# Kernel tuning notes

Measured on AMD Instinct MI355X. Metric: run time of the kernel, lower is better.

The kernel has to match this reference:

```python
import jax, jax.numpy as jnp
import numpy as np

V, N, C, H, W = 4, 65536, 128, 512, 512
M_POOL, K, DH = 1024, 5, 128


def setup_inputs() -> dict:
    key = jax.random.key(0)
    ks = jax.random.split(key, 6)
    points = jax.random.normal(ks[0], (N, 3), dtype=jnp.float32) * 0.3  # human-scale pcd near origin
    zbuffer = 2.0 + jax.random.uniform(ks[1], (V, 1, H, W), dtype=jnp.float32)  # depth ~ camera distance
    feat_map = jax.random.normal(ks[2], (V, C, H, W), dtype=jnp.float32) * 0.1
    image = jax.random.uniform(ks[3], (V, 3, H, W), dtype=jnp.float32)
    # cameras: identity rotation, small x-baseline, looking at origin from z=2.5
    R = jnp.tile(jnp.eye(3, dtype=jnp.float32)[None], (V, 1, 1))
    t = jnp.stack([jnp.array([0.1 * v - 0.15, 0.0, 2.5], dtype=jnp.float32) for v in range(V)])
    extr = jnp.concatenate([R, t[:, :, None]], axis=-1)  # [V,3,4]
    intr = jnp.tile(jnp.array([[700.0, 0.0, W / 2], [0.0, 700.0, H / 2], [0.0, 0.0, 1.0]], dtype=jnp.float32)[None], (V, 1, 1))
    W1 = jax.random.normal(ks[4], (C + 1, DH), dtype=jnp.float32) * 0.05
    b1 = jnp.zeros((DH,), dtype=jnp.float32)
    w2 = jax.random.normal(ks[5], (DH, 1), dtype=jnp.float32) * 0.05
    return dict(points=points, extr=extr, intr=intr, zbuffer=zbuffer,
                feat_map=feat_map, image=image, W1=W1, b1=b1, w2=w2)


def _bilinear(img, u, v):
    """Zero-padded bilinear sample. img [C,H,W]; u,v [N] pixel coords -> [N,C]."""
    Cc, Hh, Ww = img.shape
    u0f = jnp.floor(u); v0f = jnp.floor(v)
    du = u - u0f; dv = v - v0f
    u0 = u0f.astype(jnp.int32); v0 = v0f.astype(jnp.int32)
    out = jnp.zeros((Cc, u.shape[0]), dtype=img.dtype)
    for vi, ui, w in ((v0, u0, (1 - du) * (1 - dv)), (v0, u0 + 1, du * (1 - dv)),
                      (v0 + 1, u0, (1 - du) * dv), (v0 + 1, u0 + 1, du * dv)):
        valid = ((vi >= 0) & (vi < Hh) & (ui >= 0) & (ui < Ww)).astype(img.dtype)
        vals = img[:, jnp.clip(vi, 0, Hh - 1), jnp.clip(ui, 0, Ww - 1)]  # [C,N]
        out = out + vals * (w * valid)[None]
    return out.T  # [N,C]


def _project(points, extr, intr):
    cam = jnp.einsum('vij,nj->vni', extr[:, :, :3], points) + extr[:, None, :, 3]  # [V,N,3]
    depth = cam[..., 2]  # [V,N]
    pix = jnp.einsum('vij,vnj->vni', intr, cam)
    u = pix[..., 0] / (pix[..., 2] + 1e-9)
    v = pix[..., 1] / (pix[..., 2] + 1e-9)
    return u, v, depth


def reference(points, extr, intr, zbuffer, feat_map, image, W1, b1, w2):
    u, v, depth = _project(points, extr, intr)
    sample = jax.vmap(_bilinear)  # over V views
    zbuf = sample(zbuffer, u, v)[..., 0]  # [V,N] sampled z-buffer (0 outside frame)
    out_mask = jnp.any(zbuf == 0.0, axis=0)  # [N] point missing in some view
    # --- KNN inverse-distance zbuf replacement (torch.no_grad block) ---
    pts_sg = jax.lax.stop_gradient(points)
    zbuf_sg = jax.lax.stop_gradient(zbuf)
    cand = pts_sg[:M_POOL]                       # candidate in-point pool
    cand_bad = out_mask[:M_POOL]
    d2 = jnp.sum((pts_sg[:, None, :] - cand[None, :, :]) ** 2, axis=-1)  # [N,M]
    d2 = jnp.where(cand_bad[None, :], jnp.inf, d2)
    negd, idx = jax.lax.top_k(-d2, K)            # K nearest candidates
    dists = jnp.sqrt(jnp.maximum(-negd, 0.0))
    disp = 1.0 / (dists + 1e-8)
    wknn = disp / (jnp.sum(disp, -1, keepdims=True) + 1e-12)  # [N,K]
    replace = jnp.sum(zbuf_sg[:, idx] * wknn[None], -1)       # [V,N]
    zbuf = jnp.where(out_mask[None], replace, zbuf)
    # --- visibility ---
    vis = 1.0 - jnp.abs(zbuf - depth) / (zbuf + 1e-9)  # [V,N]
    # --- multi-view projector sampling + attention fusion (MVF) ---
    feat_s = sample(feat_map, u, v)  # [V,N,C]
    rgb_s = sample(image, u, v)      # [V,N,3]
    x = jnp.concatenate([feat_s, vis[..., None]], -1)          # [V,N,C+1]
    h = jax.nn.relu(jnp.einsum('vnc,cd->vnd', x, W1) + b1)     # [V,N,DH]
    attn = jax.nn.softmax(jnp.einsum('vnd,do->vno', h, w2), axis=0)  # softmax over views
    feat = jnp.sum(attn * feat_s, axis=0)  # [N,C]
    rgb = jnp.sum(attn * rgb_s, axis=0)    # [N,3]
    return jnp.concatenate([feat, rgb], axis=-1)  # [N,C+3]
```

## Files before the change

kernel.cpp:

```cpp
#include <hip/hip_runtime.h>
#include <math.h>

#define NV 4
#define NPT 65536
#define NC 128
#define IMH 512
#define IMW 512
#define MPOOL 1024
#define NDH 128
#define KNN 5
#define NB 8
#define OUTC 131

typedef unsigned int uint32;
typedef unsigned short ushort16;
typedef __attribute__((ext_vector_type(8))) short short8v;
typedef __attribute__((ext_vector_type(4))) float float4v;

__device__ inline ushort16 f2bf(float f) {
    uint32 u = __float_as_uint(f);
    u += 0x7fffu + ((u >> 16) & 1u);
    return (ushort16)(u >> 16);
}
__device__ inline float bflo(uint32 a) { return __uint_as_float(a << 16); }
__device__ inline float bfhi(uint32 a) { return __uint_as_float(a & 0xffff0000u); }
__device__ inline float bf1(ushort16 a) { return __uint_as_float(((uint32)a) << 16); }

__global__ void k_wprep(const float* __restrict__ W1, uint4* __restrict__ Bf,
                        int* __restrict__ counter) {
    int idx = blockIdx.x * blockDim.x + threadIdx.x;
    if (idx == 0) *counter = 0;
    if (idx >= 5 * 8 * 64) return;
    int l = idx & 63, t = (idx >> 6) & 7, kb = idx >> 9;
    int d = t * 16 + (l & 15);
    uint32 w[4];
#pragma unroll
    for (int p = 0; p < 4; ++p) {
        uint32 lohi = 0;
#pragma unroll
        for (int h = 0; h < 2; ++h) {
            int j = p * 2 + h;
            int k = kb * 32 + (l >> 4) * 8 + j;
            float wv = (k < NC + 1) ? W1[k * NDH + d] : 0.f;
            lohi |= ((uint32)f2bf(wv)) << (16 * h);
        }
        w[p] = lohi;
    }
    Bf[idx] = make_uint4(w[0], w[1], w[2], w[3]);
}

__global__ __launch_bounds__(256)
void k_prep(const float* __restrict__ pts, const float* __restrict__ extr,
            const float* __restrict__ intr, const float* __restrict__ zbuffer,
            float* __restrict__ uarr, float* __restrict__ varr,
            float* __restrict__ darr, float* __restrict__ zarr,
            int* __restrict__ mask, int* __restrict__ list,
            int* __restrict__ counter) {
    int n = blockIdx.x * blockDim.x + threadIdx.x;
    if (n >= NPT) return;
    float p0 = pts[3 * n], p1 = pts[3 * n + 1], p2 = pts[3 * n + 2];
    int msk = 0;
#pragma unroll
    for (int v = 0; v < NV; ++v) {
        const float* e = extr + v * 12;
        float c0 = e[0] * p0 + e[1] * p1 + e[2] * p2 + e[3];
        float c1 = e[4] * p0 + e[5] * p1 + e[6] * p2 + e[7];
        float c2 = e[8] * p0 + e[9] * p1 + e[10] * p2 + e[11];
        const float* kk = intr + v * 9;
        float x0 = kk[0] * c0 + kk[1] * c1 + kk[2] * c2;
        float x1 = kk[3] * c0 + kk[4] * c1 + kk[5] * c2;
        float x2 = kk[6] * c0 + kk[7] * c1 + kk[8] * c2;
        float uu = x0 / (x2 + 1e-9f);
        float vv = x1 / (x2 + 1e-9f);
        int vn = v * NPT + n;
        uarr[vn] = uu; varr[vn] = vv; darr[vn] = c2;

        const float* img = zbuffer + (size_t)v * IMH * IMW;
        float u0f = floorf(uu), v0f = floorf(vv);
        float du = uu - u0f, dv = vv - v0f;
        int iu0 = (int)u0f, iv0 = (int)v0f;
        float w00 = (1.f - du) * (1.f - dv);
        float w01 = du * (1.f - dv);
        float w10 = (1.f - du) * dv;
        float w11 = du * dv;
        int iu0c = min(max(iu0, 0), IMW - 1), iu1c = min(max(iu0 + 1, 0), IMW - 1);
        int iv0c = min(max(iv0, 0), IMH - 1), iv1c = min(max(iv0 + 1, 0), IMH - 1);
        float m00 = (iu0 >= 0 && iu0 < IMW && iv0 >= 0 && iv0 < IMH) ? w00 : 0.f;
        float m01 = (iu0 + 1 >= 0 && iu0 + 1 < IMW && iv0 >= 0 && iv0 < IMH) ? w01 : 0.f;
        float m10 = (iu0 >= 0 && iu0 < IMW && iv0 + 1 >= 0 && iv0 + 1 < IMH) ? w10 : 0.f;
        float m11 = (iu0 + 1 >= 0 && iu0 + 1 < IMW && iv0 + 1 >= 0 && iv0 + 1 < IMH) ? w11 : 0.f;
        float z = img[iv0c * IMW + iu0c] * m00 + img[iv0c * IMW + iu1c] * m01 +
                  img[iv1c * IMW + iu0c] * m10 + img[iv1c * IMW + iu1c] * m11;
        zarr[vn] = z;
        msk |= (z == 0.f);
    }
    mask[n] = msk;
    if (msk) {
        int pos = atomicAdd(counter, 1);
        list[pos] = n;
    }
}

__global__ __launch_bounds__(256)
void k_knn_c(const float* __restrict__ pts, const int* __restrict__ mask,
             const int* __restrict__ list, const int* __restrict__ counter,
             float* __restrict__ zarr) {
    __shared__ float cx[MPOOL], cy[MPOOL], cz[MPOOL];
    int count = *counter;
    if ((int)blockIdx.x * 256 >= count) return;
    for (int m = threadIdx.x; m < MPOOL; m += 256) {
        int bad = mask[m];
        cx[m] = bad ? INFINITY : pts[3 * m];
        cy[m] = pts[3 * m + 1];
        cz[m] = pts[3 * m + 2];
    }
    __syncthreads();
    int i = blockIdx.x * 256 + threadIdx.x;
    if (i >= count) return;
    int n = list[i];
    float px = pts[3 * n], py = pts[3 * n + 1], pz = pts[3 * n + 2];
    float bd[KNN];
    int bi[KNN];
#pragma unroll
    for (int k = 0; k < KNN; ++k) { bd[k] = INFINITY; bi[k] = 0; }
    for (int m = 0; m < MPOOL; ++m) {
        float dx = px - cx[m];
        float dy = py - cy[m];
        float dz = pz - cz[m];
        float d = dx * dx + dy * dy + dz * dz;
        int id = m;
#pragma unroll
        for (int k = 0; k < KNN; ++k) {
            if (d < bd[k]) {
                float td = bd[k]; int ti = bi[k];
                bd[k] = d; bi[k] = id;
                d = td; id = ti;
            }
        }
    }
    float disp[KNN];
    float s = 0.f;
#pragma unroll
    for (int k = 0; k < KNN; ++k) {
        float dist = sqrtf(fmaxf(bd[k], 0.f));
        disp[k] = 1.f / (dist + 1e-8f);
        s += disp[k];
    }
    float inv = 1.f / (s + 1e-12f);
#pragma unroll
    for (int v = 0; v < NV; ++v) {
        float r = 0.f;
#pragma unroll
        for (int k = 0; k < KNN; ++k) r += zarr[v * NPT + bi[k]] * (disp[k] * inv);
        zarr[v * NPT + n] = r;
    }
}

__global__ __launch_bounds__(256)
void k_tfeat(const float* __restrict__ feat, ushort16* __restrict__ tfeat) {
    __shared__ ushort16 tile[128][130];
    int bid = blockIdx.x;
    int xt = bid & 3;
    int y = (bid >> 2) & 511;
    int v = bid >> 11;
    int x0 = xt * 128;
    int lane = threadIdx.x & 63, wave = threadIdx.x >> 6;
    int half = lane >> 5, l5 = lane & 31;
    const size_t HW = (size_t)IMH * IMW;
    const float* src = feat + (size_t)v * NC * HW + (size_t)y * IMW + x0;
#pragma unroll
    for (int i = 0; i < 16; ++i) {
        int c = i * 8 + wave * 2 + half;
        float4 val = *(const float4*)(src + (size_t)c * HW + l5 * 4);
        int px = l5 * 4;
        tile[px + 0][c] = f2bf(val.x);
        tile[px + 1][c] = f2bf(val.y);
        tile[px + 2][c] = f2bf(val.z);
        tile[px + 3][c] = f2bf(val.w);
    }
    __syncthreads();
    uint32* dst = (uint32*)tfeat + ((size_t)v * HW + (size_t)y * IMW + x0) * 64;
#pragma unroll
    for (int i = 0; i < 32; ++i) {
        int pix = i * 4 + wave;
        uint32 val = *(const uint32*)&tile[pix][2 * lane];
        dst[(size_t)pix * 64 + lane] = val;
    }
}

__global__ __launch_bounds__(128)
void k_fused_m(const float* __restrict__ uarr, const float* __restrict__ varr,
               const float* __restrict__ darr, const float* __restrict__ zarr,
               const ushort16* __restrict__ tfeat, const float* __restrict__ image,
               const uint4* __restrict__ Bf, const float* __restrict__ b1,
               const float* __restrict__ w2, float* __restrict__ out) {
    const int tid = threadIdx.x;
    const int n0 = blockIdx.x * NB;
    const size_t HW = (size_t)IMH * IMW;
    __shared__ ushort16 fs[32][168];
    __shared__ float rgbs[32][3];
    __shared__ int po[32][4];
    __shared__ float pm[32][4];
    __shared__ float sc[32];
    __shared__ float red[32][2];

    {
        int q = tid >> 2, corner = tid & 3;
        int nb = q >> 2, v = q & 3;
        int vn = v * NPT + n0 + nb;
        float uu = uarr[vn], vv = varr[vn];
        float u0f = floorf(uu), v0f = floorf(vv);
        float du = uu - u0f, dv = vv - v0f;
        int iu0 = (int)u0f, iv0 = (int)v0f;
        float w00 = (1.f - du) * (1.f - dv);
        float w01 = du * (1.f - dv);
        float w10 = (1.f - du) * dv;
        float w11 = du * dv;
        int iu0c = min(max(iu0, 0), IMW - 1), iu1c = min(max(iu0 + 1, 0), IMW - 1);
        int iv0c = min(max(iv0, 0), IMH - 1), iv1c = min(max(iv0 + 1, 0), IMH - 1);
        float m00 = (iu0 >= 0 && iu0 < IMW && iv0 >= 0 && iv0 < IMH) ? w00 : 0.f;
        float m01 = (iu0 + 1 < IMW && iu0 + 1 >= 0 && iv0 >= 0 && iv0 < IMH) ? w01 : 0.f;
        float m10 = (iu0 >= 0 && iu0 < IMW && iv0 + 1 < IMH && iv0 + 1 >= 0) ? w10 : 0.f;
        float m11 = (iu0 + 1 < IMW && iu0 + 1 >= 0 && iv0 + 1 < IMH && iv0 + 1 >= 0) ? w11 : 0.f;
        int iuc, ivc;
        float mm;
        if (corner == 0)      { ivc = iv0c; iuc = iu0c; mm = m00; }
        else if (corner == 1) { ivc = iv0c; iuc = iu1c; mm = m01; }
        else if (corner == 2) { ivc = iv1c; iuc = iu0c; mm = m10; }
        else                  { ivc = iv1c; iuc = iu1c; mm = m11; }
        int oo = ivc * IMW + iuc;
        po[q][corner] = oo;
        pm[q][corner] = mm;
        const float* ib = image + (size_t)v * 3 * HW + oo;
        float cr = ib[0] * mm, cg = ib[HW] * mm, cb = ib[2 * HW] * mm;
        cr += __shfl_xor(cr, 1); cr += __shfl_xor(cr, 2);
        cg += __shfl_xor(cg, 1); cg += __shfl_xor(cg, 2);
        cb += __shfl_xor(cb, 1); cb += __shfl_xor(cb, 2);
        if (corner == 0) {
            rgbs[q][0] = cr; rgbs[q][1] = cg; rgbs[q][2] = cb;
            float z = zarr[vn], dd = darr[vn];
            float vis = 1.f - fabsf(z - dd) / (z + 1e-9f);
            fs[q][128] = f2bf(vis);
        }
        for (int k = 129 + corner; k < 168; k += 4) fs[q][k] = 0;
    }
    __syncthreads();

    const uint32* T = (const uint32*)tfeat;
    {
        int wv = tid >> 6, l = tid & 63;
        int ql = l >> 4, g = l & 15;
#pragma unroll
        for (int i = 0; i < 4; ++i) {
            int q = i * 8 + wv * 4 + ql;
            int v = q & 3;
            const uint32* Bv = T + (size_t)v * HW * 64;
            float a0 = 0.f, a1 = 0.f, a2 = 0.f, a3 = 0.f;
            float a4 = 0.f, a5 = 0.f, a6 = 0.f, a7 = 0.f;
#pragma unroll
            for (int k = 0; k < 4; ++k) {
                uint4 A = *(const uint4*)(Bv + (size_t)po[q][k] * 64 + g * 4);
                float m = pm[q][k];
                a0 += bflo(A.x) * m; a1 += bfhi(A.x) * m;
                a2 += bflo(A.y) * m; a3 += bfhi(A.y) * m;
                a4 += bflo(A.z) * m; a5 += bfhi(A.z) * m;
                a6 += bflo(A.w) * m; a7 += bfhi(A.w) * m;
            }
            uint4 r;
            r.x = (uint32)f2bf(a0) | ((uint32)f2bf(a1) << 16);
            r.y = (uint32)f2bf(a2) | ((uint32)f2bf(a3) << 16);
            r.z = (uint32)f2bf(a4) | ((uint32)f2bf(a5) << 16);
            r.w = (uint32)f2bf(a6) | ((uint32)f2bf(a7) << 16);
            *(uint4*)&fs[q][g * 8] = r;
        }
    }
    __syncthreads();

    const int l = tid & 63, w = tid >> 6;
    const int col = l & 15, kg = l >> 4;
    float4v acc[2][4];
#pragma unroll
    for (int g = 0; g < 2; ++g)
#pragma unroll
        for (int t = 0; t < 4; ++t) acc[g][t] = (float4v){0.f, 0.f, 0.f, 0.f};
#pragma unroll
    for (int kb = 0; kb < 5; ++kb) {
        short8v a0 = *(const short8v*)&fs[col][kb * 32 + kg * 8];
        short8v a1 = *(const short8v*)&fs[16 + col][kb * 32 + kg * 8];
#pragma unroll
        for (int tt = 0; tt < 4; ++tt) {
            int t = w * 4 + tt;
            short8v bv = *(const short8v*)&Bf[(kb * 8 + t) * 64 + l];
            acc[0][tt] = __builtin_amdgcn_mfma_f32_16x16x32_bf16(a0, bv, acc[0][tt], 0, 0, 0);
            acc[1][tt] = __builtin_amdgcn_mfma_f32_16x16x32_bf16(a1, bv, acc[1][tt], 0, 0, 0);
        }
    }
    float bias[4], w2v[4];
#pragma unroll
    for (int tt = 0; tt < 4; ++tt) {
        int d = (w * 4 + tt) * 16 + col;
        bias[tt] = b1[d];
        w2v[tt] = w2[d];
    }
    float p[2][4] = {{0.f, 0.f, 0.f, 0.f}, {0.f, 0.f, 0.f, 0.f}};
#pragma unroll
    for (int g = 0; g < 2; ++g)
#pragma unroll
        for (int tt = 0; tt < 4; ++tt)
#pragma unroll
            for (int r = 0; r < 4; ++r)
                p[g][r] += fmaxf(acc[g][tt][r] + bias[tt], 0.f) * w2v[tt];
#pragma unroll
    for (int m = 1; m < 16; m <<= 1)
#pragma unroll
        for (int g = 0; g < 2; ++g)
#pragma unroll
            for (int r = 0; r < 4; ++r) p[g][r] += __shfl_xor(p[g][r], m);
    if (col == 0) {
#pragma unroll
        for (int g = 0; g < 2; ++g)
#pragma unroll
            for (int r = 0; r < 4; ++r) red[g * 16 + kg * 4 + r][w] = p[g][r];
    }
    __syncthreads();
    if (tid < 32) sc[tid] = red[tid][0] + red[tid][1];
    __syncthreads();
    if (tid < NB) {
        float s0 = sc[tid * 4 + 0], s1 = sc[tid * 4 + 1];
        float s2 = sc[tid * 4 + 2], s3 = sc[tid * 4 + 3];
        float mx = fmaxf(fmaxf(s0, s1), fmaxf(s2, s3));
        float e0 = expf(s0 - mx), e1 = expf(s1 - mx);
        float e2 = expf(s2 - mx), e3 = expf(s3 - mx);
        float inv = 1.f / (e0 + e1 + e2 + e3);
        sc[tid * 4 + 0] = e0 * inv; sc[tid * 4 + 1] = e1 * inv;
        sc[tid * 4 + 2] = e2 * inv; sc[tid * 4 + 3] = e3 * inv;
    }
    __syncthreads();

#pragma unroll
    for (int nb = 0; nb < NB; ++nb) {
        int n = n0 + nb;
        float f = 0.f;
#pragma unroll
        for (int v = 0; v < NV; ++v) f += sc[nb * 4 + v] * bf1(fs[nb * 4 + v][tid]);
        out[(size_t)n * OUTC + tid] = f;
        if (tid < 3) {
            float r = 0.f;
#pragma unroll
            for (int v = 0; v < NV; ++v) r += sc[nb * 4 + v] * rgbs[nb * 4 + v][tid];
            out[(size_t)n * OUTC + NC + tid] = r;
        }
    }
}

__global__ __launch_bounds__(128)
void k_fused_d(const float* __restrict__ uarr, const float* __restrict__ varr,
               const float* __restrict__ darr, const float* __restrict__ zarr,
               const float* __restrict__ feat, const float* __restrict__ image,
               const float* __restrict__ W1, const float* __restrict__ b1,
               const float* __restrict__ w2, float* __restrict__ out) {
    const int tid = threadIdx.x;
    const int n0 = blockIdx.x * 4;
    __shared__ float fs[4][NV][NC];
    __shared__ float rgbs[4][NV][3];
    __shared__ float sc[4][NV];
    __shared__ float red[4][NV][2];
    float vis[4][NV];

#pragma unroll
    for (int nb = 0; nb < 4; ++nb) {
        int n = n0 + nb;
#pragma unroll
        for (int v = 0; v < NV; ++v) {
            int vn = v * NPT + n;
            float uu = uarr[vn], vv = varr[vn];
            float u0f = floorf(uu), v0f = floorf(vv);
            float du = uu - u0f, dv = vv - v0f;
            int iu0 = (int)u0f, iv0 = (int)v0f;
            float w00 = (1.f - du) * (1.f - dv);
            float w01 = du * (1.f - dv);
            float w10 = (1.f - du) * dv;
            float w11 = du * dv;
            int iu0c = min(max(iu0, 0), IMW - 1), iu1c = min(max(iu0 + 1, 0), IMW - 1);
            int iv0c = min(max(iv0, 0), IMH - 1), iv1c = min(max(iv0 + 1, 0), IMH - 1);
            float m00 = (iu0 >= 0 && iu0 < IMW && iv0 >= 0 && iv0 < IMH) ? w00 : 0.f;
            float m01 = (iu0 + 1 < IMW && iu0 + 1 >= 0 && iv0 >= 0 && iv0 < IMH) ? w01 : 0.f;
            float m10 = (iu0 >= 0 && iu0 < IMW && iv0 + 1 < IMH && iv0 + 1 >= 0) ? w10 : 0.f;
            float m11 = (iu0 + 1 < IMW && iu0 + 1 >= 0 && iv0 + 1 < IMH && iv0 + 1 >= 0) ? w11 : 0.f;
            int o00 = iv0c * IMW + iu0c, o01 = iv0c * IMW + iu1c;
            int o10 = iv1c * IMW + iu0c, o11 = iv1c * IMW + iu1c;
            const float* base = feat + ((size_t)(v * NC + tid)) * IMH * IMW;
            fs[nb][v][tid] = base[o00] * m00 + base[o01] * m01 +
                             base[o10] * m10 + base[o11] * m11;
            if (tid < 3) {
                const float* ib = image + ((size_t)(v * 3 + tid)) * IMH * IMW;
                rgbs[nb][v][tid] = ib[o00] * m00 + ib[o01] * m01 +
                                   ib[o10] * m10 + ib[o11] * m11;
            }
            float z = zarr[vn], dd = darr[vn];
            vis[nb][v] = 1.f - fabsf(z - dd) / (z + 1e-9f);
        }
    }
    __syncthreads();

    float h[4][NV];
    float bv = b1[tid];
#pragma unroll
    for (int nb = 0; nb < 4; ++nb)
#pragma unroll
        for (int v = 0; v < NV; ++v) h[nb][v] = bv;
    for (int c = 0; c < NC; ++c) {
        float w = W1[c * NDH + tid];
#pragma unroll
        for (int nb = 0; nb < 4; ++nb)
#pragma unroll
            for (int v = 0; v < NV; ++v) h[nb][v] = fmaf(fs[nb][v][c], w, h[nb][v]);
    }
    {
        float w = W1[NC * NDH + tid];
#pragma unroll
        for (int nb = 0; nb < 4; ++nb)
#pragma unroll
            for (int v = 0; v < NV; ++v) h[nb][v] = fmaf(vis[nb][v], w, h[nb][v]);
    }
    float w2t = w2[tid];
    int lane = tid & 63, wave = tid >> 6;
#pragma unroll
    for (int nb = 0; nb < 4; ++nb) {
#pragma unroll
        for (int v = 0; v < NV; ++v) {
            float p = fmaxf(h[nb][v], 0.f) * w2t;
#pragma unroll
            for (int off = 32; off > 0; off >>= 1) p += __shfl_down(p, off);
            if (lane == 0) red[nb][v][wave] = p;
        }
    }
    __syncthreads();
    if (tid < 16) {
        int nb = tid >> 2, v = tid & 3;
        sc[nb][v] = red[nb][v][0] + red[nb][v][1];
    }
    __syncthreads();
    if (tid < 4) {
        float s0 = sc[tid][0], s1 = sc[tid][1], s2 = sc[tid][2], s3 = sc[tid][3];
        float mx = fmaxf(fmaxf(s0, s1), fmaxf(s2, s3));
        float e0 = expf(s0 - mx), e1 = expf(s1 - mx);
        float e2 = expf(s2 - mx), e3 = expf(s3 - mx);
        float inv = 1.f / (e0 + e1 + e2 + e3);
        sc[tid][0] = e0 * inv; sc[tid][1] = e1 * inv;
        sc[tid][2] = e2 * inv; sc[tid][3] = e3 * inv;
    }
    __syncthreads();
#pragma unroll
    for (int nb = 0; nb < 4; ++nb) {
        int n = n0 + nb;
        float f = 0.f;
#pragma unroll
        for (int v = 0; v < NV; ++v) f += sc[nb][v] * fs[nb][v][tid];
        out[(size_t)n * OUTC + tid] = f;
        if (tid < 3) {
            float r = 0.f;
#pragma unroll
            for (int v = 0; v < NV; ++v) r += sc[nb][v] * rgbs[nb][v][tid];
            out[(size_t)n * OUTC + NC + tid] = r;
        }
    }
}

extern "C" void kernel_launch(void* const* d_in, const int* in_sizes, int n_in,
                              void* d_out, int out_size, void* d_ws, size_t ws_size,
                              hipStream_t stream) {
    const float* pts = (const float*)d_in[0];
    const float* extr = (const float*)d_in[1];
    const float* intr = (const float*)d_in[2];
    const float* zbuffer = (const float*)d_in[3];
    const float* feat = (const float*)d_in[4];
    const float* image = (const float*)d_in[5];
    const float* W1 = (const float*)d_in[6];
    const float* b1 = (const float*)d_in[7];
    const float* w2 = (const float*)d_in[8];
    float* out = (float*)d_out;

    const size_t VN = (size_t)NV * NPT;
    float* uarr = (float*)d_ws;
    float* varr = uarr + VN;
    float* darr = varr + VN;
    float* zarr = darr + VN;
    int* mask = (int*)(zarr + VN);
    int* list = mask + NPT;
    int* counter = list + NPT;
    uint4* Bf = (uint4*)(counter + 16);
    char* after = (char*)(Bf + 5 * 8 * 64);
    ushort16* tfeat = (ushort16*)after;
    size_t need = (size_t)((char*)tfeat - (char*)d_ws) + (size_t)NV * IMH * IMW * NC * 2;

    k_wprep<<<10, 256, 0, stream>>>(W1, Bf, counter);
    k_prep<<<NPT / 256, 256, 0, stream>>>(pts, extr, intr, zbuffer,
                                          uarr, varr, darr, zarr,
                                          mask, list, counter);
    k_knn_c<<<NPT / 256, 256, 0, stream>>>(pts, mask, list, counter, zarr);

    if (ws_size >= need) {
        k_tfeat<<<NV * 512 * 4, 256, 0, stream>>>(feat, tfeat);
        k_fused_m<<<NPT / NB, 128, 0, stream>>>(uarr, varr, darr, zarr, tfeat, image,
                                                Bf, b1, w2, out);
    } else {
        k_fused_d<<<NPT / 4, 128, 0, stream>>>(uarr, varr, darr, zarr, feat, image,
                                               W1, b1, w2, out);
    }
}
```

Measured before the change: 472.2 us.

## Split fused sampling kernel into per-view transpose+MLP passes and a final fusion kernel

Restructures the fast path so each view is transposed to bf16 and then immediately sampled and scored by an MLP kernel, one view at a time. The aim is to keep each view's transposed feature map hot in the large cache while it is gathered, instead of gathering across all four views' 128 MB of transposed data. Sampled features and scores go to new workspace buffers, and a final kernel does the softmax, the weighted sum and the RGB sampling. This adds global writes and reads of the intermediate features (about 64 MB bf16 each way), extra kernel launches, and a larger workspace requirement. If the workspace is too small, the code falls back to the direct kernel.

```diff
diff --git a/kernel.cpp b/kernel.cpp
--- a/kernel.cpp
+++ b/kernel.cpp
@@ -9,7 +9,6 @@
 #define MPOOL 1024
 #define NDH 128
 #define KNN 5
-#define NB 8
 #define OUTC 131
 
 typedef unsigned int uint32;
@@ -157,12 +156,12 @@
 }
 
 __global__ __launch_bounds__(256)
-void k_tfeat(const float* __restrict__ feat, ushort16* __restrict__ tfeat) {
+void k_tfeat_v(const float* __restrict__ feat, ushort16* __restrict__ tfeat,
+               int v) {
     __shared__ ushort16 tile[128][130];
     int bid = blockIdx.x;
     int xt = bid & 3;
-    int y = (bid >> 2) & 511;
-    int v = bid >> 11;
+    int y = bid >> 2;
     int x0 = xt * 128;
     int lane = threadIdx.x & 63, wave = threadIdx.x >> 6;
     int half = lane >> 5, l5 = lane & 31;
@@ -189,20 +188,142 @@
 }
 
 __global__ __launch_bounds__(128)
-void k_fused_m(const float* __restrict__ uarr, const float* __restrict__ varr,
-               const float* __restrict__ darr, const float* __restrict__ zarr,
-               const ushort16* __restrict__ tfeat, const float* __restrict__ image,
-               const uint4* __restrict__ Bf, const float* __restrict__ b1,
-               const float* __restrict__ w2, float* __restrict__ out) {
+void k_mlp_v(const float* __restrict__ uarr, const float* __restrict__ varr,
+             const float* __restrict__ darr, const float* __restrict__ zarr,
+             const ushort16* __restrict__ tfeat, const uint4* __restrict__ Bf,
+             const float* __restrict__ b1, const float* __restrict__ w2,
+             ushort16* __restrict__ fsb, float* __restrict__ sbuf, int v) {
     const int tid = threadIdx.x;
-    const int n0 = blockIdx.x * NB;
+    const int n0 = blockIdx.x * 32;
     const size_t HW = (size_t)IMH * IMW;
     __shared__ ushort16 fs[32][168];
-    __shared__ float rgbs[32][3];
     __shared__ int po[32][4];
     __shared__ float pm[32][4];
+    __shared__ float red[32][2];
+
+    {
+        int q = tid >> 2, corner = tid & 3;
+        int vn = v * NPT + n0 + q;
+        float uu = uarr[vn], vv = varr[vn];
+        float u0f = floorf(uu), v0f = floorf(vv);
+        float du = uu - u0f, dv = vv - v0f;
+        int iu0 = (int)u0f, iv0 = (int)v0f;
+        float w00 = (1.f - du) * (1.f - dv);
+        float w01 = du * (1.f - dv);
+        float w10 = (1.f - du) * dv;
+        float w11 = du * dv;
+        int iu0c = min(max(iu0, 0), IMW - 1), iu1c = min(max(iu0 + 1, 0), IMW - 1);
+        int iv0c = min(max(iv0, 0), IMH - 1), iv1c = min(max(iv0 + 1, 0), IMH - 1);
+        float m00 = (iu0 >= 0 && iu0 < IMW && iv0 >= 0 && iv0 < IMH) ? w00 : 0.f;
+        float m01 = (iu0 + 1 < IMW && iu0 + 1 >= 0 && iv0 >= 0 && iv0 < IMH) ? w01 : 0.f;
+        float m10 = (iu0 >= 0 && iu0 < IMW && iv0 + 1 < IMH && iv0 + 1 >= 0) ? w10 : 0.f;
+        float m11 = (iu0 + 1 < IMW && iu0 + 1 >= 0 && iv0 + 1 < IMH && iv0 + 1 >= 0) ? w11 : 0.f;
+        int iuc, ivc;
+        float mm;
+        if (corner == 0)      { ivc = iv0c; iuc = iu0c; mm = m00; }
+        else if (corner == 1) { ivc = iv0c; iuc = iu1c; mm = m01; }
+        else if (corner == 2) { ivc = iv1c; iuc = iu0c; mm = m10; }
+        else                  { ivc = iv1c; iuc = iu1c; mm = m11; }
+        po[q][corner] = ivc * IMW + iuc;
+        pm[q][corner] = mm;
+        if (corner == 0) {
+            float z = zarr[vn], dd = darr[vn];
+            float vis = 1.f - fabsf(z - dd) / (z + 1e-9f);
+            fs[q][128] = f2bf(vis);
+        }
+        for (int k = 129 + corner; k < 168; k += 4) fs[q][k] = 0;
+    }
+    __syncthreads();
+
+    const uint32* T = (const uint32*)tfeat + (size_t)v * HW * 64;
+    uint32* F = (uint32*)fsb + ((size_t)v * NPT + n0) * 64;
+    {
+        int wv = tid >> 6, l = tid & 63;
+        int ql = l >> 4, g = l & 15;
+#pragma unroll
+        for (int i = 0; i < 4; ++i) {
+            int q = i * 8 + wv * 4 + ql;
+            float a0 = 0.f, a1 = 0.f, a2 = 0.f, a3 = 0.f;
+            float a4 = 0.f, a5 = 0.f, a6 = 0.f, a7 = 0.f;
+#pragma unroll
+            for (int k = 0; k < 4; ++k) {
+                uint4 A = *(const uint4*)(T + (size_t)po[q][k] * 64 + g * 4);
+                float m = pm[q][k];
+                a0 += bflo(A.x) * m; a1 += bfhi(A.x) * m;
+                a2 += bflo(A.y) * m; a3 += bfhi(A.y) * m;
+                a4 += bflo(A.z) * m; a5 += bfhi(A.z) * m;
+                a6 += bflo(A.w) * m; a7 += bfhi(A.w) * m;
+            }
+            uint4 r;
+            r.x = (uint32)f2bf(a0) | ((uint32)f2bf(a1) << 16);
+            r.y = (uint32)f2bf(a2) | ((uint32)f2bf(a3) << 16);
+            r.z = (uint32)f2bf(a4) | ((uint32)f2bf(a5) << 16);
+            r.w = (uint32)f2bf(a6) | ((uint32)f2bf(a7) << 16);
+            *(uint4*)&fs[q][g * 8] = r;
+            *(uint4*)(F + (size_t)q * 64 + g * 4) = r;
+        }
+    }
+    __syncthreads();
+
+    const int l = tid & 63, w = tid >> 6;
+    const int col = l & 15, kg = l >> 4;
+    float4v acc[2][4];
+#pragma unroll
+    for (int g = 0; g < 2; ++g)
+#pragma unroll
+        for (int t = 0; t < 4; ++t) acc[g][t] = (float4v){0.f, 0.f, 0.f, 0.f};
+#pragma unroll
+    for (int kb = 0; kb < 5; ++kb) {
+        short8v a0 = *(const short8v*)&fs[col][kb * 32 + kg * 8];
+        short8v a1 = *(const short8v*)&fs[16 + col][kb * 32 + kg * 8];
+#pragma unroll
+        for (int tt = 0; tt < 4; ++tt) {
+            int t = w * 4 + tt;
+            short8v bv = *(const short8v*)&Bf[(kb * 8 + t) * 64 + l];
+            acc[0][tt] = __builtin_amdgcn_mfma_f32_16x16x32_bf16(a0, bv, acc[0][tt], 0, 0, 0);
+            acc[1][tt] = __builtin_amdgcn_mfma_f32_16x16x32_bf16(a1, bv, acc[1][tt], 0, 0, 0);
+        }
+    }
+    float bias[4], w2v[4];
+#pragma unroll
+    for (int tt = 0; tt < 4; ++tt) {
+        int d = (w * 4 + tt) * 16 + col;
+        bias[tt] = b1[d];
+        w2v[tt] = w2[d];
+    }
+    float p[2][4] = {{0.f, 0.f, 0.f, 0.f}, {0.f, 0.f, 0.f, 0.f}};
+#pragma unroll
+    for (int g = 0; g < 2; ++g)
+#pragma unroll
+        for (int tt = 0; tt < 4; ++tt)
+#pragma unroll
+            for (int r = 0; r < 4; ++r)
+                p[g][r] += fmaxf(acc[g][tt][r] + bias[tt], 0.f) * w2v[tt];
+#pragma unroll
+    for (int m = 1; m < 16; m <<= 1)
+#pragma unroll
+        for (int g = 0; g < 2; ++g)
+#pragma unroll
+            for (int r = 0; r < 4; ++r) p[g][r] += __shfl_xor(p[g][r], m);
+    if (col == 0) {
+#pragma unroll
+        for (int g = 0; g < 2; ++g)
+#pragma unroll
+            for (int r = 0; r < 4; ++r) red[g * 16 + kg * 4 + r][w] = p[g][r];
+    }
+    __syncthreads();
+    if (tid < 32) sbuf[v * NPT + n0 + tid] = red[tid][0] + red[tid][1];
+}
+
+__global__ __launch_bounds__(128)
+void k_final(const float* __restrict__ uarr, const float* __restrict__ varr,
+             const float* __restrict__ image, const ushort16* __restrict__ fsb,
+             const float* __restrict__ sbuf, float* __restrict__ out) {
+    const int tid = threadIdx.x;
+    const int n0 = blockIdx.x * 8;
+    const size_t HW = (size_t)IMH * IMW;
+    __shared__ float rgbs[32][3];
     __shared__ float sc[32];
-    __shared__ float red[32][2];
 
     {
         int q = tid >> 2, corner = tid & 3;
@@ -229,8 +350,6 @@
         else if (corner == 2) { ivc = iv1c; iuc = iu0c; mm = m10; }
         else                  { ivc = iv1c; iuc = iu1c; mm = m11; }
         int oo = ivc * IMW + iuc;
-        po[q][corner] = oo;
-        pm[q][corner] = mm;
         const float* ib = image + (size_t)v * 3 * HW + oo;
         float cr = ib[0] * mm, cg = ib[HW] * mm, cb = ib[2 * HW] * mm;
         cr += __shfl_xor(cr, 1); cr += __shfl_xor(cr, 2);
@@ -238,96 +357,13 @@
         cb += __shfl_xor(cb, 1); cb += __shfl_xor(cb, 2);
         if (corner == 0) {
             rgbs[q][0] = cr; rgbs[q][1] = cg; rgbs[q][2] = cb;
-            float z = zarr[vn], dd = darr[vn];
-            float vis = 1.f - fabsf(z - dd) / (z + 1e-9f);
-            fs[q][128] = f2bf(vis);
-        }
-        for (int k = 129 + corner; k < 168; k += 4) fs[q][k] = 0;
-    }
-    __syncthreads();
-
-    const uint32* T = (const uint32*)tfeat;
-    {
-        int wv = tid >> 6, l = tid & 63;
-        int ql = l >> 4, g = l & 15;
-#pragma unroll
-        for (int i = 0; i < 4; ++i) {
-            int q = i * 8 + wv * 4 + ql;
-            int v = q & 3;
-            const uint32* Bv = T + (size_t)v * HW * 64;
-            float a0 = 0.f, a1 = 0.f, a2 = 0.f, a3 = 0.f;
-            float a4 = 0.f, a5 = 0.f, a6 = 0.f, a7 = 0.f;
-#pragma unroll
-            for (int k = 0; k < 4; ++k) {
-                uint4 A = *(const uint4*)(Bv + (size_t)po[q][k] * 64 + g * 4);
-                float m = pm[q][k];
-                a0 += bflo(A.x) * m; a1 += bfhi(A.x) * m;
-                a2 += bflo(A.y) * m; a3 += bfhi(A.y) * m;
-                a4 += bflo(A.z) * m; a5 += bfhi(A.z) * m;
-                a6 += bflo(A.w) * m; a7 += bfhi(A.w) * m;
-            }
-            uint4 r;
-            r.x = (uint32)f2bf(a0) | ((uint32)f2bf(a1) << 16);
-            r.y = (uint32)f2bf(a2) | ((uint32)f2bf(a3) << 16);
-            r.z = (uint32)f2bf(a4) | ((uint32)f2bf(a5) << 16);
-            r.w = (uint32)f2bf(a6) | ((uint32)f2bf(a7) << 16);
-            *(uint4*)&fs[q][g * 8] = r;
-        }
-    }
-    __syncthreads();
-
-    const int l = tid & 63, w = tid >> 6;
-    const int col = l & 15, kg = l >> 4;
-    float4v acc[2][4];
-#pragma unroll
-    for (int g = 0; g < 2; ++g)
-#pragma unroll
-        for (int t = 0; t < 4; ++t) acc[g][t] = (float4v){0.f, 0.f, 0.f, 0.f};
-#pragma unroll
-    for (int kb = 0; kb < 5; ++kb) {
-        short8v a0 = *(const short8v*)&fs[col][kb * 32 + kg * 8];
-        short8v a1 = *(const short8v*)&fs[16 + col][kb * 32 + kg * 8];
-#pragma unroll
-        for (int tt = 0; tt < 4; ++tt) {
-            int t = w * 4 + tt;
-            short8v bv = *(const short8v*)&Bf[(kb * 8 + t) * 64 + l];
-            acc[0][tt] = __builtin_amdgcn_mfma_f32_16x16x32_bf16(a0, bv, acc[0][tt], 0, 0, 0);
-            acc[1][tt] = __builtin_amdgcn_mfma_f32_16x16x32_bf16(a1, bv, acc[1][tt], 0, 0, 0);
-        }
-    }
-    float bias[4], w2v[4];
-#pragma unroll
-    for (int tt = 0; tt < 4; ++tt) {
-        int d = (w * 4 + tt) * 16 + col;
-        bias[tt] = b1[d];
-        w2v[tt] = w2[d];
-    }
-    float p[2][4] = {{0.f, 0.f, 0.f, 0.f}, {0.f, 0.f, 0.f, 0.f}};
-#pragma unroll
-    for (int g = 0; g < 2; ++g)
-#pragma unroll
-        for (int tt = 0; tt < 4; ++tt)
-#pragma unroll
-            for (int r = 0; r < 4; ++r)
-                p[g][r] += fmaxf(acc[g][tt][r] + bias[tt], 0.f) * w2v[tt];
-#pragma unroll
-    for (int m = 1; m < 16; m <<= 1)
-#pragma unroll
-        for (int g = 0; g < 2; ++g)
-#pragma unroll
-            for (int r = 0; r < 4; ++r) p[g][r] += __shfl_xor(p[g][r], m);
-    if (col == 0) {
-#pragma unroll
-        for (int g = 0; g < 2; ++g)
-#pragma unroll
-            for (int r = 0; r < 4; ++r) red[g * 16 + kg * 4 + r][w] = p[g][r];
-    }
-    __syncthreads();
-    if (tid < 32) sc[tid] = red[tid][0] + red[tid][1];
-    __syncthreads();
-    if (tid < NB) {
-        float s0 = sc[tid * 4 + 0], s1 = sc[tid * 4 + 1];
-        float s2 = sc[tid * 4 + 2], s3 = sc[tid * 4 + 3];
+        }
+    }
+    __syncthreads();
+    if (tid < 8) {
+        int n = n0 + tid;
+        float s0 = sbuf[0 * NPT + n], s1 = sbuf[1 * NPT + n];
+        float s2 = sbuf[2 * NPT + n], s3 = sbuf[3 * NPT + n];
         float mx = fmaxf(fmaxf(s0, s1), fmaxf(s2, s3));
         float e0 = expf(s0 - mx), e1 = expf(s1 - mx);
         float e2 = expf(s2 - mx), e3 = expf(s3 - mx);
@@ -338,11 +374,12 @@
     __syncthreads();
 
 #pragma unroll
-    for (int nb = 0; nb < NB; ++nb) {
+    for (int nb = 0; nb < 8; ++nb) {
         int n = n0 + nb;
         float f = 0.f;
 #pragma unroll
-        for (int v = 0; v < NV; ++v) f += sc[nb * 4 + v] * bf1(fs[nb * 4 + v][tid]);
+        for (int v = 0; v < NV; ++v)
+            f += sc[nb * 4 + v] * bf1(fsb[((size_t)v * NPT + n) * 128 + tid]);
         out[(size_t)n * OUTC + tid] = f;
         if (tid < 3) {
             float r = 0.f;
@@ -490,8 +527,9 @@
     int* list = mask + NPT;
     int* counter = list + NPT;
     uint4* Bf = (uint4*)(counter + 16);
-    char* after = (char*)(Bf + 5 * 8 * 64);
-    ushort16* tfeat = (ushort16*)after;
+    float* sbuf = (float*)(Bf + 5 * 8 * 64);
+    ushort16* fsb = (ushort16*)(sbuf + VN);
+    ushort16* tfeat = fsb + VN * 128;
     size_t need = (size_t)((char*)tfeat - (char*)d_ws) + (size_t)NV * IMH * IMW * NC * 2;
 
     k_wprep<<<10, 256, 0, stream>>>(W1, Bf, counter);
@@ -501,9 +539,12 @@
     k_knn_c<<<NPT / 256, 256, 0, stream>>>(pts, mask, list, counter, zarr);
 
     if (ws_size >= need) {
-        k_tfeat<<<NV * 512 * 4, 256, 0, stream>>>(feat, tfeat);
-        k_fused_m<<<NPT / NB, 128, 0, stream>>>(uarr, varr, darr, zarr, tfeat, image,
-                                                Bf, b1, w2, out);
+        for (int v = 0; v < NV; ++v) {
+            k_tfeat_v<<<512 * 4, 256, 0, stream>>>(feat, tfeat, v);
+            k_mlp_v<<<NPT / 32, 128, 0, stream>>>(uarr, varr, darr, zarr, tfeat,
+                                                  Bf, b1, w2, fsb, sbuf, v);
+        }
+        k_final<<<NPT / 8, 128, 0, stream>>>(uarr, varr, image, fsb, sbuf, out);
     } else {
         k_fused_d<<<NPT / 4, 128, 0, stream>>>(uarr, varr, darr, zarr, feat, image,
                                                W1, b1, w2, out);
```

Result: slower. 510.3 us (+8.1%).
